# Kernel optimization log

Measured on AMD Instinct MI355X. Metric: run time of the kernel, lower is better.

Reference implementation:

```python
import jax, jax.numpy as jnp
import numpy as np

SIZE = 784          # number of MPS sites (pixels)
D = 32              # bond dimension
EMB_D = 2           # local feature dim, embedding x -> [1-x, x]
NUM_LABELS = 10
LABEL_SITE = SIZE // 2
BATCH = 128
INIT_STD = 0.01     # matches default 'random_eye' init


def setup_inputs() -> dict:
    key = jax.random.key(0)
    k1, k2, k3 = jax.random.split(key, 3)
    # raw pixel values in [0,1] so the affine embedding is valid
    batch_input = jax.random.uniform(k1, (BATCH, SIZE), dtype=jnp.float32)
    eye = jnp.eye(D, dtype=jnp.float32)
    # 'random_eye' init: identity (broadcast over site & physical dims) + small noise.
    # Keeps the 784-long matrix chain numerically well-conditioned.
    core_tensors = eye[None, :, None, :] + INIT_STD * jax.random.normal(
        k2, (SIZE, D, EMB_D, D), dtype=jnp.float32)
    label_tensor = eye[:, None, :] + INIT_STD * jax.random.normal(
        k3, (D, NUM_LABELS, D), dtype=jnp.float32)
    return {"batch_input": batch_input,
            "core_tensors": core_tensors,
            "label_tensor": label_tensor}


def _chain_matmul(mats):
    """Ordered product M_0 @ M_1 @ ... @ M_{n-1} via log-depth pairwise tree.
    mats: [B, n, D, D] -> [B, D, D]. n is static, so the Python while is fine."""
    while mats.shape[1] > 1:
        n = mats.shape[1]
        half = n // 2
        prod = jnp.matmul(mats[:, 0:2 * half:2], mats[:, 1:2 * half:2])
        if n % 2:
            prod = jnp.concatenate([prod, mats[:, -1:]], axis=1)
        mats = prod
    return mats[:, 0]


def reference(batch_input, core_tensors, label_tensor):
    # embedding_map: x -> [1-x, x]                                  [B, S, d]
    emb = jnp.stack([1.0 - batch_input, batch_input], axis=-1)
    # _contract_batch_input: per-site matrices M[b,s] = sum_d core[s,:,d,:]*emb[b,s,d]
    mats = jnp.einsum('sadc,bsd->bsac', core_tensors, emb)       # [B, S, D, D]
    left = _chain_matmul(mats[:, :LABEL_SITE])                    # [B, D, D]
    right = _chain_matmul(mats[:, LABEL_SITE:])                   # [B, D, D]
    # periodic bc: out[b,l] = trace(left @ T_l @ right)
    return jnp.einsum('bij,jlk,bki->bl', left, label_tensor, right)  # [B, num_labels]
```

## Files before the change

### kernel.cpp

```cpp
#include <hip/hip_runtime.h>
#include <stdint.h>

typedef float f32x16 __attribute__((ext_vector_type(16)));
typedef short bf16x8 __attribute__((ext_vector_type(8)));
typedef uint32_t u32;

#define SIZE 784
#define NLBL 10
#define LABEL_SITE 392
#define BATCH 128
#define NSEG 56
#define SEGLEN 14
#define BIW 2


__device__ inline u32 cvt_pk(float a, float b) {
  u32 r;
  asm("v_cvt_pk_bf16_f32 %0, %1, %2" : "=v"(r) : "v"(a), "v"(b));
  return r;
}

__device__ inline void split_pack(const float s[8], u32 hi[4], u32 lo[4]) {
#pragma unroll
  for (int p = 0; p < 4; ++p) {
    u32 h = cvt_pk(s[2 * p], s[2 * p + 1]);
    hi[p] = h;
    float he = __uint_as_float(h << 16);
    float ho = __uint_as_float(h & 0xffff0000u);
    lo[p] = cvt_pk(s[2 * p] - he, s[2 * p + 1] - ho);
  }
}

__device__ inline f32x16 mfma_bb(const u32 (&a)[4], const u32 (&b)[4], f32x16 c) {
  union U { u32 u[4]; bf16x8 v; };
  U A, B;
#pragma unroll
  for (int i = 0; i < 4; ++i) { A.u[i] = a[i]; B.u[i] = b[i]; }
  return __builtin_amdgcn_mfma_f32_32x32x16_bf16(A.v, B.v, c, 0, 0, 0);
}

__device__ inline f32x16 ident_acc(int lane) {
  const int gam = lane & 31, hib = lane >> 5;
  f32x16 a;
#pragma unroll
  for (int reg = 0; reg < 16; ++reg) {
    int rho = (reg & 3) + 8 * (reg >> 2) + 4 * hib;
    a[reg] = (rho == gam) ? 1.0f : 0.0f;
  }
  return a;
}

__device__ inline f32x16 chain_step(const u32 (&Ah)[2][4], const u32 (&Al)[2][4],
                                    f32x16 acc, int hib) {
  float pr[16];
#pragma unroll
  for (int q = 0; q < 16; ++q) pr[q] = __shfl_xor(acc[q], 32, 64);
  u32 Bh[2][4], Bl[2][4];
#pragma unroll
  for (int t = 0; t < 2; ++t) {
    float slot[8];
#pragma unroll
    for (int j = 0; j < 4; ++j) slot[j] = hib ? pr[8 * t + j + 4] : acc[8 * t + j];
#pragma unroll
    for (int j = 4; j < 8; ++j) slot[j] = hib ? acc[8 * t + j] : pr[8 * t + j - 4];
    split_pack(slot, Bh[t], Bl[t]);
  }
  f32x16 r;
#pragma unroll
  for (int i = 0; i < 16; ++i) r[i] = 0.0f;
  r = mfma_bb(Al[0], Bl[0], r);
  r = mfma_bb(Al[1], Bl[1], r);
  r = mfma_bb(Ah[0], Bl[0], r);
  r = mfma_bb(Ah[1], Bl[1], r);
  r = mfma_bb(Al[0], Bh[0], r);
  r = mfma_bb(Al[1], Bh[1], r);
  r = mfma_bb(Ah[0], Bh[0], r);
  r = mfma_bb(Ah[1], Bh[1], r);
  return r;
}

__device__ inline void store_afrag(float* dst, f32x16 acc, int lane) {
  const int gam = lane & 31, hib = lane >> 5;
  const int h = gam >> 4, j = gam & 7, b5 = (gam >> 3) & 1;
#pragma unroll
  for (int reg = 0; reg < 16; ++reg) {
    int rho = (reg & 3) + 8 * (reg >> 2) + 4 * hib;
    int lp = rho + 32 * b5;
    dst[h * 512 + lp * 8 + j] = acc[reg];
  }
}

__device__ inline void load_split_afrag(const float* src, int lane,
                                        u32 (&Ah)[2][4], u32 (&Al)[2][4]) {
#pragma unroll
  for (int h = 0; h < 2; ++h) {
    const float4* p = (const float4*)(src + h * 512 + lane * 8);
    float4 q0 = p[0], q1 = p[1];
    float v[8] = {q0.x, q0.y, q0.z, q0.w, q1.x, q1.y, q1.z, q1.w};
    split_pack(v, Ah[h], Al[h]);
  }
}

__global__ __launch_bounds__(256) void mps_phase1(const float* __restrict__ input,
                                                  const float* __restrict__ core,
                                                  float* __restrict__ wsA) {
  const int tid = threadIdx.x;
  const int w = tid >> 6, lane = tid & 63;
  const int r = lane & 31, hib = lane >> 5;
  const int g = blockIdx.x % NSEG, c = blockIdx.x / NSEG;
  const int bi0 = c * (4 * BIW) + w * BIW;

  f32x16 acc[BIW];
#pragma unroll
  for (int b = 0; b < BIW; ++b) acc[b] = ident_acc(lane);

  for (int i = 0; i < SEGLEN; ++i) {
    const int ci = g * SEGLEN + i;
    const int s = (LABEL_SITE + ci) % SIZE;
    const float* cs = core + (size_t)s * 2048 + r;
    float c0v[16], dv[16];
#pragma unroll
    for (int t = 0; t < 2; ++t)
#pragma unroll
      for (int j = 0; j < 8; ++j) {
        const int kk = 16 * t + 8 * hib + j;
        float a0 = cs[kk * 64];
        float a1 = cs[kk * 64 + 32];
        c0v[8 * t + j] = a0;
        dv[8 * t + j] = a1 - a0;
      }
#pragma unroll
    for (int b = 0; b < BIW; ++b) {
      const float x = input[(size_t)(bi0 + b) * SIZE + s];
      u32 Ah[2][4], Al[2][4];
#pragma unroll
      for (int t = 0; t < 2; ++t) {
        float m[8];
#pragma unroll
        for (int j = 0; j < 8; ++j) m[j] = fmaf(x, dv[8 * t + j], c0v[8 * t + j]);
        split_pack(m, Ah[t], Al[t]);
      }
      acc[b] = chain_step(Ah, Al, acc[b], hib);
    }
  }
#pragma unroll
  for (int b = 0; b < BIW; ++b) {
    float* dst = wsA + ((size_t)(bi0 + b) * NSEG + g) * 1024;
    store_afrag(dst, acc[b], lane);
  }
}

__global__ __launch_bounds__(256) void mps_phase2a(const float* __restrict__ wsA,
                                                   float* __restrict__ wsB) {
  const int tid = threadIdx.x;
  const int w = tid >> 6, lane = tid & 63;
  const int wid = blockIdx.x * 4 + w;
  const int bi = wid & 127, gg = wid >> 7;
  f32x16 acc = ident_acc(lane);
  for (int g = gg * 8; g < gg * 8 + 8; ++g) {
    u32 Ah[2][4], Al[2][4];
    load_split_afrag(wsA + ((size_t)bi * NSEG + g) * 1024, lane, Ah, Al);
    acc = chain_step(Ah, Al, acc, lane >> 5);
  }
  store_afrag(wsB + ((size_t)bi * 7 + gg) * 1024, acc, lane);
}

__global__ __launch_bounds__(256) void mps_phase2b(const float* __restrict__ wsB,
                                                   const float* __restrict__ label,
                                                   float* __restrict__ out) {
  const int tid = threadIdx.x;
  const int w = tid >> 6, lane = tid & 63;
  const int bi = blockIdx.x * 4 + w;
  const int gam = lane & 31, hib = lane >> 5;
  f32x16 acc = ident_acc(lane);
  for (int gg = 0; gg < 7; ++gg) {
    u32 Ah[2][4], Al[2][4];
    load_split_afrag(wsB + ((size_t)bi * 7 + gg) * 1024, lane, Ah, Al);
    acc = chain_step(Ah, Al, acc, hib);
  }
  float part[NLBL];
#pragma unroll
  for (int l = 0; l < NLBL; ++l) part[l] = 0.0f;
#pragma unroll
  for (int reg = 0; reg < 16; ++reg) {
    const int rho = (reg & 3) + 8 * (reg >> 2) + 4 * hib;
    const float wv = acc[reg];
    const float* tp = label + rho * (NLBL * 32) + gam;
#pragma unroll
    for (int l = 0; l < NLBL; ++l) part[l] = fmaf(tp[l * 32], wv, part[l]);
  }
#pragma unroll
  for (int l = 0; l < NLBL; ++l) {
#pragma unroll
    for (int mask = 32; mask >= 1; mask >>= 1)
      part[l] += __shfl_xor(part[l], mask, 64);
  }
  if (lane == 0) {
#pragma unroll
    for (int l = 0; l < NLBL; ++l) out[bi * NLBL + l] = part[l];
  }
}

extern "C" void kernel_launch(void* const* d_in, const int* in_sizes, int n_in,
                              void* d_out, int out_size, void* d_ws, size_t ws_size,
                              hipStream_t stream) {
  const float* input = (const float*)d_in[0];
  const float* core  = (const float*)d_in[1];
  const float* label = (const float*)d_in[2];
  float* out = (float*)d_out;
  float* wsA = (float*)d_ws;
  float* wsB = wsA + (size_t)BATCH * NSEG * 1024;

  mps_phase1<<<dim3(NSEG * (BATCH / (4 * BIW))), dim3(256), 0, stream>>>(input, core, wsA);
  mps_phase2a<<<dim3(224), dim3(256), 0, stream>>>(wsA, wsB);
  mps_phase2b<<<dim3(32), dim3(256), 0, stream>>>(wsB, label, out);
}
```

Baseline: 69.16 us.

## Precompute split-bf16 core fragments and use linearity in x per site

Adds a precompute kernel that converts core slices (c0 and c1-c0) into hi/lo bf16 MFMA fragments once per call. Phase1 then loads these fragments directly and computes C0·P and D·P separately, combining them as x*rd+rc, since the site matrix is linear in x. This removes per-batch conversion and the split of site matrices, but doubles the MFMA count per step. It also drops the lo*lo MFMA term from the three-term split product, which costs some precision. Further changes: one batch per wave, an option of 112 segments when the workspace is large enough, and interleaved shuffles in build_b.

```diff
diff --git a/kernel.cpp b/kernel.cpp
--- a/kernel.cpp
+++ b/kernel.cpp
@@ -4,14 +4,13 @@
 typedef float f32x16 __attribute__((ext_vector_type(16)));
 typedef short bf16x8 __attribute__((ext_vector_type(8)));
 typedef uint32_t u32;
+typedef uint32_t u32x4 __attribute__((ext_vector_type(4)));
 
 #define SIZE 784
 #define NLBL 10
 #define LABEL_SITE 392
 #define BATCH 128
-#define NSEG 56
-#define SEGLEN 14
-#define BIW 2
+#define PRE_ELEMS (SIZE * 2 * 64 * 4)
 
 
 __device__ inline u32 cvt_pk(float a, float b) {
@@ -19,15 +18,15 @@
   asm("v_cvt_pk_bf16_f32 %0, %1, %2" : "=v"(r) : "v"(a), "v"(b));
   return r;
 }
+__device__ inline float lo16f(u32 h) { return __uint_as_float(h << 16); }
+__device__ inline float hi16f(u32 h) { return __uint_as_float(h & 0xffff0000u); }
 
 __device__ inline void split_pack(const float s[8], u32 hi[4], u32 lo[4]) {
 #pragma unroll
   for (int p = 0; p < 4; ++p) {
     u32 h = cvt_pk(s[2 * p], s[2 * p + 1]);
     hi[p] = h;
-    float he = __uint_as_float(h << 16);
-    float ho = __uint_as_float(h & 0xffff0000u);
-    lo[p] = cvt_pk(s[2 * p] - he, s[2 * p + 1] - ho);
+    lo[p] = cvt_pk(s[2 * p] - lo16f(h), s[2 * p + 1] - hi16f(h));
   }
 }
 
@@ -38,6 +37,13 @@
   for (int i = 0; i < 4; ++i) { A.u[i] = a[i]; B.u[i] = b[i]; }
   return __builtin_amdgcn_mfma_f32_32x32x16_bf16(A.v, B.v, c, 0, 0, 0);
 }
+__device__ inline f32x16 mfma_v4(u32x4 a, const u32 (&b)[4], f32x16 c) {
+  union UA { u32x4 u; bf16x8 v; } A; A.u = a;
+  union UB { u32 u[4]; bf16x8 v; } B;
+#pragma unroll
+  for (int i = 0; i < 4; ++i) B.u[i] = b[i];
+  return __builtin_amdgcn_mfma_f32_32x32x16_bf16(A.v, B.v, c, 0, 0, 0);
+}
 
 __device__ inline f32x16 ident_acc(int lane) {
   const int gam = lane & 31, hib = lane >> 5;
@@ -50,32 +56,33 @@
   return a;
 }
 
+__device__ inline void build_b(const f32x16& acc, int hib, int t,
+                               u32 (&Bh)[4], u32 (&Bl)[4]) {
+  float slot[8];
+#pragma unroll
+  for (int j = 0; j < 4; ++j) {
+    const int q1 = 8 * t + j, q2 = q1 + 4;
+    float z = hib ? acc[q1] : acc[q2];
+    float wv = __shfl_xor(z, 32, 64);
+    slot[j]     = hib ? wv : acc[q1];
+    slot[j + 4] = hib ? acc[q2] : wv;
+  }
+  split_pack(slot, Bh, Bl);
+}
+
 __device__ inline f32x16 chain_step(const u32 (&Ah)[2][4], const u32 (&Al)[2][4],
                                     f32x16 acc, int hib) {
-  float pr[16];
-#pragma unroll
-  for (int q = 0; q < 16; ++q) pr[q] = __shfl_xor(acc[q], 32, 64);
-  u32 Bh[2][4], Bl[2][4];
+  f32x16 r;
+#pragma unroll
+  for (int q = 0; q < 16; ++q) r[q] = 0.0f;
 #pragma unroll
   for (int t = 0; t < 2; ++t) {
-    float slot[8];
-#pragma unroll
-    for (int j = 0; j < 4; ++j) slot[j] = hib ? pr[8 * t + j + 4] : acc[8 * t + j];
-#pragma unroll
-    for (int j = 4; j < 8; ++j) slot[j] = hib ? acc[8 * t + j] : pr[8 * t + j - 4];
-    split_pack(slot, Bh[t], Bl[t]);
-  }
-  f32x16 r;
-#pragma unroll
-  for (int i = 0; i < 16; ++i) r[i] = 0.0f;
-  r = mfma_bb(Al[0], Bl[0], r);
-  r = mfma_bb(Al[1], Bl[1], r);
-  r = mfma_bb(Ah[0], Bl[0], r);
-  r = mfma_bb(Ah[1], Bl[1], r);
-  r = mfma_bb(Al[0], Bh[0], r);
-  r = mfma_bb(Al[1], Bh[1], r);
-  r = mfma_bb(Ah[0], Bh[0], r);
-  r = mfma_bb(Ah[1], Bh[1], r);
+    u32 Bh[4], Bl[4];
+    build_b(acc, hib, t, Bh, Bl);
+    r = mfma_bb(Al[t], Bh, r);
+    r = mfma_bb(Ah[t], Bl, r);
+    r = mfma_bb(Ah[t], Bh, r);
+  }
   return r;
 }
 
@@ -101,65 +108,93 @@
   }
 }
 
-__global__ __launch_bounds__(256) void mps_phase1(const float* __restrict__ input,
-                                                  const float* __restrict__ core,
-                                                  float* __restrict__ wsA) {
-  const int tid = threadIdx.x;
-  const int w = tid >> 6, lane = tid & 63;
+__global__ __launch_bounds__(256) void mps_precomp(const float* __restrict__ core,
+                                                   u32* __restrict__ pc0h,
+                                                   u32* __restrict__ pc0l,
+                                                   u32* __restrict__ pdh,
+                                                   u32* __restrict__ pdl) {
+  const int tid = threadIdx.x;
+  const int w = tid >> 6, lane = tid & 63;
+  const int task = blockIdx.x * 4 + w;
+  const int s = task >> 1, t = task & 1;
   const int r = lane & 31, hib = lane >> 5;
-  const int g = blockIdx.x % NSEG, c = blockIdx.x / NSEG;
-  const int bi0 = c * (4 * BIW) + w * BIW;
-
-  f32x16 acc[BIW];
-#pragma unroll
-  for (int b = 0; b < BIW; ++b) acc[b] = ident_acc(lane);
-
-  for (int i = 0; i < SEGLEN; ++i) {
-    const int ci = g * SEGLEN + i;
-    const int s = (LABEL_SITE + ci) % SIZE;
-    const float* cs = core + (size_t)s * 2048 + r;
-    float c0v[16], dv[16];
-#pragma unroll
-    for (int t = 0; t < 2; ++t)
-#pragma unroll
-      for (int j = 0; j < 8; ++j) {
-        const int kk = 16 * t + 8 * hib + j;
-        float a0 = cs[kk * 64];
-        float a1 = cs[kk * 64 + 32];
-        c0v[8 * t + j] = a0;
-        dv[8 * t + j] = a1 - a0;
-      }
-#pragma unroll
-    for (int b = 0; b < BIW; ++b) {
-      const float x = input[(size_t)(bi0 + b) * SIZE + s];
-      u32 Ah[2][4], Al[2][4];
-#pragma unroll
-      for (int t = 0; t < 2; ++t) {
-        float m[8];
-#pragma unroll
-        for (int j = 0; j < 8; ++j) m[j] = fmaf(x, dv[8 * t + j], c0v[8 * t + j]);
-        split_pack(m, Ah[t], Al[t]);
-      }
-      acc[b] = chain_step(Ah, Al, acc[b], hib);
+  const float* cs = core + (size_t)s * 2048 + r;
+  u32 wc0h[4], wc0l[4], wdh[4], wdl[4];
+#pragma unroll
+  for (int p = 0; p < 4; ++p) {
+    const int k0 = 16 * t + 8 * hib + 2 * p;
+    float a0 = cs[k0 * 64],       a1 = cs[(k0 + 1) * 64];
+    float b0 = cs[k0 * 64 + 32],  b1 = cs[(k0 + 1) * 64 + 32];
+    float d0 = b0 - a0, d1 = b1 - a1;
+    u32 h = cvt_pk(a0, a1);
+    wc0h[p] = h;
+    wc0l[p] = cvt_pk(a0 - lo16f(h), a1 - hi16f(h));
+    u32 gg = cvt_pk(d0, d1);
+    wdh[p] = gg;
+    wdl[p] = cvt_pk(d0 - lo16f(gg), d1 - hi16f(gg));
+  }
+  const size_t base = ((size_t)task * 64 + lane) * 4;
+  *(u32x4*)(pc0h + base) = *(u32x4*)wc0h;
+  *(u32x4*)(pc0l + base) = *(u32x4*)wc0l;
+  *(u32x4*)(pdh  + base) = *(u32x4*)wdh;
+  *(u32x4*)(pdl  + base) = *(u32x4*)wdl;
+}
+
+__global__ __launch_bounds__(256, 4) void mps_phase1(
+    const float* __restrict__ input,
+    const u32* __restrict__ pc0h, const u32* __restrict__ pc0l,
+    const u32* __restrict__ pdh,  const u32* __restrict__ pdl,
+    float* __restrict__ wsA, int nseg, int seglen) {
+  const int tid = threadIdx.x;
+  const int w = tid >> 6, lane = tid & 63;
+  const int hib = lane >> 5;
+  const int g = blockIdx.x % nseg, c = blockIdx.x / nseg;
+  const int bi = c * 4 + w;
+
+  f32x16 acc = ident_acc(lane);
+  f32x16 z16;
+#pragma unroll
+  for (int q = 0; q < 16; ++q) z16[q] = 0.0f;
+
+  const int ci0 = g * seglen;
+  for (int i = 0; i < seglen; ++i) {
+    int s = LABEL_SITE + ci0 + i;
+    if (s >= SIZE) s -= SIZE;
+    const float x = input[(size_t)bi * SIZE + s];
+    f32x16 rc = z16, rd = z16;
+#pragma unroll
+    for (int t = 0; t < 2; ++t) {
+      const size_t base = ((size_t)(s * 2 + t) * 64 + lane) * 4;
+      u32x4 Ac0h = *(const u32x4*)(pc0h + base);
+      u32x4 Ac0l = *(const u32x4*)(pc0l + base);
+      u32x4 Adh  = *(const u32x4*)(pdh + base);
+      u32x4 Adl  = *(const u32x4*)(pdl + base);
+      u32 Bh[4], Bl[4];
+      build_b(acc, hib, t, Bh, Bl);
+      rd = mfma_v4(Adl, Bh, rd);
+      rd = mfma_v4(Adh, Bl, rd);
+      rd = mfma_v4(Adh, Bh, rd);
+      rc = mfma_v4(Ac0l, Bh, rc);
+      rc = mfma_v4(Ac0h, Bl, rc);
+      rc = mfma_v4(Ac0h, Bh, rc);
     }
-  }
-#pragma unroll
-  for (int b = 0; b < BIW; ++b) {
-    float* dst = wsA + ((size_t)(bi0 + b) * NSEG + g) * 1024;
-    store_afrag(dst, acc[b], lane);
-  }
+#pragma unroll
+    for (int q = 0; q < 16; ++q) acc[q] = fmaf(x, rd[q], rc[q]);
+  }
+  store_afrag(wsA + ((size_t)bi * nseg + g) * 1024, acc, lane);
 }
 
 __global__ __launch_bounds__(256) void mps_phase2a(const float* __restrict__ wsA,
-                                                   float* __restrict__ wsB) {
+                                                   float* __restrict__ wsB,
+                                                   int nseg, int GG) {
   const int tid = threadIdx.x;
   const int w = tid >> 6, lane = tid & 63;
   const int wid = blockIdx.x * 4 + w;
   const int bi = wid & 127, gg = wid >> 7;
   f32x16 acc = ident_acc(lane);
-  for (int g = gg * 8; g < gg * 8 + 8; ++g) {
+  for (int g = gg * GG; g < gg * GG + GG; ++g) {
     u32 Ah[2][4], Al[2][4];
-    load_split_afrag(wsA + ((size_t)bi * NSEG + g) * 1024, lane, Ah, Al);
+    load_split_afrag(wsA + ((size_t)bi * nseg + g) * 1024, lane, Ah, Al);
     acc = chain_step(Ah, Al, acc, lane >> 5);
   }
   store_afrag(wsB + ((size_t)bi * 7 + gg) * 1024, acc, lane);
@@ -208,10 +243,23 @@
   const float* core  = (const float*)d_in[1];
   const float* label = (const float*)d_in[2];
   float* out = (float*)d_out;
-  float* wsA = (float*)d_ws;
-  float* wsB = wsA + (size_t)BATCH * NSEG * 1024;
-
-  mps_phase1<<<dim3(NSEG * (BATCH / (4 * BIW))), dim3(256), 0, stream>>>(input, core, wsA);
-  mps_phase2a<<<dim3(224), dim3(256), 0, stream>>>(wsA, wsB);
+
+  u32* pc0h = (u32*)d_ws;
+  u32* pc0l = pc0h + PRE_ELEMS;
+  u32* pdh  = pc0l + PRE_ELEMS;
+  u32* pdl  = pdh + PRE_ELEMS;
+  float* wsA = (float*)(pdl + PRE_ELEMS);
+
+  const size_t need112 = ((size_t)4 * PRE_ELEMS + (size_t)BATCH * 112 * 1024 +
+                          (size_t)BATCH * 7 * 1024) * 4;
+  const int nseg = (ws_size >= need112) ? 112 : 56;
+  const int seglen = SIZE / nseg;
+  const int GG = nseg / 7;
+  float* wsB = wsA + (size_t)BATCH * nseg * 1024;
+
+  mps_precomp<<<dim3(392), dim3(256), 0, stream>>>(core, pc0h, pc0l, pdh, pdl);
+  mps_phase1<<<dim3(nseg * 32), dim3(256), 0, stream>>>(input, pc0h, pc0l, pdh, pdl,
+                                                        wsA, nseg, seglen);
+  mps_phase2a<<<dim3(224), dim3(256), 0, stream>>>(wsA, wsB, nseg, GG);
   mps_phase2b<<<dim3(32), dim3(256), 0, stream>>>(wsB, label, out);
 }
```

Result: slower. 76.64 us (+10.8%).
